# Performance work log

Hardware: AMD Instinct MI355X
Metric: run time of the kernel (lower is better)

## Reference

```python
import jax, jax.numpy as jnp
import numpy as np
from jax.scipy.special import gammaln

# NQ_IN + 4 == 2*H is required because the two kernel=1, padding=1 convs grow the
# length axis by 4 and the following nn.Linear(2H, H) acts on the length axis.
B, NQ_IN, NK, QDIM, KDIM, H = 16, 2044, 1024, 80, 256, 1024


def setup_inputs() -> dict:
    ks = jax.random.split(jax.random.key(0), 14)
    s = 0.02
    return {
        "query": jax.random.normal(ks[0], (B, NQ_IN, QDIM), jnp.float32),
        "key": jax.random.normal(ks[1], (B, NK, KDIM), jnp.float32),
        "query_lens": jnp.full((B,), 2 * H, jnp.int32),
        "key_lens": jnp.full((B,), NK, jnp.int32),
        # query branch params (Conv1d k=1 stored as (out,in); Linear as (out,in))
        "qc1_w": jax.random.normal(ks[2], (2 * H, QDIM), jnp.float32) * s,
        "qc1_b": jax.random.normal(ks[3], (2 * H,), jnp.float32) * s,
        "qc2_w": jax.random.normal(ks[4], (2 * H, 2 * H), jnp.float32) * s,
        "qc2_b": jax.random.normal(ks[5], (2 * H,), jnp.float32) * s,
        "ql_w": jax.random.normal(ks[6], (H, 2 * H), jnp.float32) * s,
        "ql_b": jax.random.normal(ks[7], (H,), jnp.float32) * s,
        # key branch params
        "kc_w": jax.random.normal(ks[8], (H, KDIM, 3), jnp.float32) * s,
        "kc_b": jax.random.normal(ks[9], (H,), jnp.float32) * s,
        "kl1_w": jax.random.normal(ks[10], (2 * H, H), jnp.float32) * s,
        "kl1_b": jax.random.normal(ks[11], (2 * H,), jnp.float32) * s,
        "kl2_w": jax.random.normal(ks[12], (H, 2 * H), jnp.float32) * s,
        "kl2_b": jax.random.normal(ks[13], (H,), jnp.float32) * s,
    }


def _log_beta_binom(query_lens, key_lens, tq, tk):
    # Standard MAS beta-binomial alignment prior over a (tq, tk) grid.
    i = jnp.arange(tq, dtype=jnp.float32)[None, :, None]
    j = jnp.arange(tk, dtype=jnp.float32)[None, None, :]
    ql = query_lens.astype(jnp.float32)[:, None, None]
    kl = key_lens.astype(jnp.float32)[:, None, None]
    a = i + 1.0
    b = jnp.maximum(ql - i, 1.0)
    n = jnp.maximum(kl - 1.0, 0.0)
    nmj = jnp.maximum(n - j, 0.0)

    def betaln(x, y):
        return gammaln(x) + gammaln(y) - gammaln(x + y)

    logp = (gammaln(n + 1.0) - gammaln(j + 1.0) - gammaln(nmj + 1.0)
            + betaln(j + a, nmj + b) - betaln(a, b))
    valid = (i < ql) & (j < kl)
    return jnp.where(valid, logp, -1e9)


def _forward(query, key, query_lens, key_lens,
             qc1_w, qc1_b, qc2_w, qc2_b, ql_w, ql_b,
             kc_w, kc_b, kl1_w, kl1_b, kl2_w, kl2_b):
    # query branch: b n c -> b c n, two k=1/p=1 convs (pad length, pointwise), Linear over LENGTH axis
    q = jnp.transpose(query, (0, 2, 1))                       # (B, QDIM, NQ_IN)
    q = jnp.pad(q, ((0, 0), (0, 0), (1, 1)))
    q = jnp.einsum('bcn,oc->bon', q, qc1_w) + qc1_b[None, :, None]   # (B, 2H, NQ_IN+2)
    q = jnp.pad(q, ((0, 0), (0, 0), (1, 1)))
    q = jnp.einsum('bcn,oc->bon', q, qc2_w) + qc2_b[None, :, None]   # (B, 2H, 2H)
    q = jnp.einsum('bcn,hn->bch', q, ql_w) + ql_b                    # (B, 2H, H) Linear on length axis

    # key branch: b n c -> b c n, Conv1d k=3 p=1, then two Linears over LENGTH axis
    k = jnp.transpose(key, (0, 2, 1))                         # (B, KDIM, NK)
    k = jax.lax.conv_general_dilated(k, kc_w, (1,), ((1, 1),),
                                     dimension_numbers=('NCH', 'OIH', 'NCH'))
    k = k + kc_b[None, :, None]                               # (B, H, NK=H)
    k = jnp.einsum('bcn,on->bco', k, kl1_w) + kl1_b           # (B, H, 2H)
    k = jnp.einsum('bco,ho->bch', k, kl2_w) + kl2_b           # (B, H, H)

    # dist = -cdist(q, k), computed via the GEMM form (same as torch.cdist mm mode)
    sq = (jnp.sum(q * q, -1)[:, :, None] + jnp.sum(k * k, -1)[:, None, :]
          - 2.0 * jnp.einsum('bnd,bmd->bnm', q, k))           # (B, 2H, H)
    dist = -jnp.sqrt(jnp.maximum(sq, 1e-12))

    prior = _log_beta_binom(query_lens, key_lens, q.shape[1], k.shape[1])
    return jax.nn.log_softmax(dist + prior, axis=-1)


def reference(query, key, query_lens, key_lens,
              qc1_w, qc1_b, qc2_w, qc2_b, ql_w, ql_b,
              kc_w, kc_b, kl1_w, kl1_b, kl2_w, kl2_b):
    return _forward(query, key, query_lens, key_lens,
                    qc1_w, qc1_b, qc2_w, qc2_b, ql_w, ql_b,
                    kc_w, kc_b, kl1_w, kl1_b, kl2_w, kl2_b)
```

## Files before the change

### kernel.cpp

```cpp
#include <hip/hip_runtime.h>
#include <math.h>

typedef unsigned short u16;
typedef float floatx4 __attribute__((ext_vector_type(4)));
typedef __bf16 bf16x8 __attribute__((ext_vector_type(8)));

#define BB   16
#define TQ   2048
#define TK   1024
#define HH   1024
#define H2   2048
#define QD   80
#define QDP  128
#define KD   256
#define NQ   2044
#define NKEY 1024

__device__ __forceinline__ u16 f2bf(float f) {
  unsigned int u = __float_as_uint(f);
  u = u + 0x7fffu + ((u >> 16) & 1u);
  return (u16)(u >> 16);
}
__device__ __forceinline__ float bf2f(u16 s) {
  return __uint_as_float(((unsigned int)s) << 16);
}

__global__ __launch_bounds__(256) void prep_all_k(
    const float* __restrict__ qc2_w, const float* __restrict__ qc1_w,
    const float* __restrict__ kl2_w, const float* __restrict__ kl1_w,
    const float* __restrict__ query, const float* __restrict__ ql_w,
    const float* __restrict__ kc_w,
    u16* __restrict__ qc2w, u16* __restrict__ qc1T, u16* __restrict__ kl2w,
    u16* __restrict__ kl1T, u16* __restrict__ qT, u16* __restrict__ qlw2,
    u16* __restrict__ kcp, float* __restrict__ tbl)
{
  long b = blockIdx.x;
  const int t = threadIdx.x;
  if (b < 16384) {
    long i = b * 256 + t; qc2w[i] = f2bf(qc2_w[i]); return;
  }
  b -= 16384;
  if (b < 1024) {
    long i = b * 256 + t;
    int c = (int)(i / H2), r = (int)(i % H2);
    qc1T[i] = (c < QD) ? f2bf(qc1_w[(long)r * QD + c]) : (u16)0; return;
  }
  b -= 1024;
  if (b < 8192) {
    long i = b * 256 + t; kl2w[i] = f2bf(kl2_w[i]); return;
  }
  b -= 8192;
  if (b < 8192) {
    long i = b * 256 + t;
    int c = (int)(i / H2), r = (int)(i % H2);
    kl1T[i] = f2bf(kl1_w[(long)r * HH + c]); return;
  }
  b -= 8192;
  if (b < 16384) {
    long i = b * 256 + t;
    int n = (int)(i & 2047);
    long rem = i >> 11;
    int c = (int)(rem % QDP);
    int bb = (int)(rem / QDP);
    qT[i] = (c < QD && n < NQ) ? f2bf(query[((long)bb * NQ + n) * QD + c]) : (u16)0; return;
  }
  b -= 16384;
  if (b < 8192) {
    long i = b * 256 + t;
    int n = (int)(i & 2047);
    int h = (int)(i >> 11);
    qlw2[i] = (n < NQ) ? f2bf(ql_w[(long)h * H2 + n + 2]) : (u16)0; return;
  }
  b -= 8192;
  if (b < 3072) {
    long i = b * 256 + t;
    int r = (int)(i % 768);
    int o = (int)(i / 768);
    int tt = r >> 8, d = r & 255;
    kcp[i] = f2bf(kc_w[((long)o * KD + d) * 3 + tt]); return;
  }
  b -= 3072;
  { int i = (int)(b * 256 + t); if (i < 8192) tbl[i] = i ? (float)lgamma((double)i) : 0.0f; }
}

__global__ __launch_bounds__(256) void fold_bias_k(
    const float* __restrict__ qc2_w, const float* __restrict__ qc1_b, const float* __restrict__ qc2_b,
    const float* __restrict__ kl2_w, const float* __restrict__ kl1_b, const float* __restrict__ kl2_b,
    const float* __restrict__ ql_w,
    float* __restrict__ bqm, float* __restrict__ bkv, float* __restrict__ s1v, float* __restrict__ s0v)
{
  const int bid = blockIdx.x, t = threadIdx.x;
  float s = 0.f;
  if (bid < H2) {
    const float* row = qc2_w + (long)bid * H2;
    for (int k = t; k < H2; k += 256) s += row[k] * qc1_b[k];
  } else if (bid < H2 + HH) {
    const float* row = kl2_w + (long)(bid - H2) * H2;
    for (int k = t; k < H2; k += 256) s += row[k] * kl1_b[k];
  } else {
    const float* row = ql_w + (long)(bid - H2 - HH) * H2;
    for (int m = 1 + t; m <= H2 - 2; m += 256) s += row[m];
  }
  __shared__ float red[256];
  red[t] = s; __syncthreads();
  for (int st = 128; st > 0; st >>= 1) { if (t < st) red[t] += red[t + st]; __syncthreads(); }
  if (!t) {
    if (bid < H2) bqm[bid] = red[0] + qc2_b[bid];
    else if (bid < H2 + HH) bkv[bid - H2] = red[0] + kl2_b[bid - H2];
    else {
      int h = bid - H2 - HH;
      s1v[h] = red[0];
      s0v[h] = ql_w[(long)h * H2] + ql_w[(long)h * H2 + H2 - 1];
    }
  }
}

__global__ __launch_bounds__(256) void rownorm2_k(const u16* __restrict__ Q, const u16* __restrict__ K3,
                                                  float* __restrict__ qn, float* __restrict__ kn) {
  const long r = blockIdx.x;
  const int t = threadIdx.x;
  const u16* row = (r < (long)BB * TQ) ? (Q + r * 1024) : (K3 + (r - (long)BB * TQ) * 1024);
  uint2 v = reinterpret_cast<const uint2*>(row)[t];
  float a0 = bf2f((u16)(v.x & 0xffff)), a1 = bf2f((u16)(v.x >> 16));
  float a2 = bf2f((u16)(v.y & 0xffff)), a3 = bf2f((u16)(v.y >> 16));
  float s = a0 * a0 + a1 * a1 + a2 * a2 + a3 * a3;
  __shared__ float red[256];
  red[t] = s; __syncthreads();
  for (int st = 128; st > 0; st >>= 1) { if (t < st) red[t] += red[t + st]; __syncthreads(); }
  if (!t) {
    if (r < (long)BB * TQ) qn[r] = red[0];
    else kn[r - (long)BB * TQ] = red[0];
  }
}


__device__ __forceinline__ void gld_lds16(const u16* g, u16* l) {
  __builtin_amdgcn_global_load_lds((const __attribute__((address_space(1))) void*)g,
                                   (__attribute__((address_space(3))) void*)l, 16, 0, 0);
}

template<int OUTF32>
__global__ __launch_bounds__(256) void gemm_bt(
    const u16* __restrict__ A, const u16* __restrict__ B, void* __restrict__ Cv,
    int M, int N, int K, int lda, int ldb, int swap,
    long sA, long sB, long sC,
    const float* __restrict__ colb, const float* __restrict__ rowb,
    const float* __restrict__ r1m, const float* __restrict__ r1n,
    const float* __restrict__ r2m, const float* __restrict__ r2n)
{
  __shared__ __align__(16) u16 As[128 * 32];
  __shared__ __align__(16) u16 Bs[128 * 32];
  const int bz = blockIdx.z;
  const int tid  = threadIdx.x;
  const int lane = tid & 63;
  const int wv = tid >> 6;
  const int wm = ((tid >> 7) & 1) * 64;
  const int wn = ((tid >> 6) & 1) * 64;
  const int m0 = (swap ? blockIdx.x : blockIdx.y) * 128;
  const int n0 = (swap ? blockIdx.y : blockIdx.x) * 128;

  const int srow = wv * 32 + (lane >> 2);
  const int scol = (lane & 3) << 3;
  const u16* ga = A + bz * sA + (long)(m0 + srow) * lda + scol;
  const u16* gb = B + bz * sB + (long)(n0 + srow) * ldb + scol;
  u16* la0 = &As[(wv * 32) * 32];
  u16* la1 = &As[(wv * 32 + 16) * 32];
  u16* lb0 = &Bs[(wv * 32) * 32];
  u16* lb1 = &Bs[(wv * 32 + 16) * 32];
  const long a16 = (long)16 * lda;
  const long b16 = (long)16 * ldb;

  floatx4 acc[4][4];
#pragma unroll
  for (int a_ = 0; a_ < 4; a_++)
#pragma unroll
    for (int b_ = 0; b_ < 4; b_++) acc[a_][b_] = (floatx4){0.f, 0.f, 0.f, 0.f};

  const int fr = lane & 15;
  const int fk = (lane >> 4) << 3;

  for (int kb = 0; kb < K; kb += 32) {
    gld_lds16(ga,       la0);
    gld_lds16(ga + a16, la1);
    gld_lds16(gb,       lb0);
    gld_lds16(gb + b16, lb1);
    ga += 32; gb += 32;
    __syncthreads();
    bf16x8 af[4], bfr[4];
#pragma unroll
    for (int mi = 0; mi < 4; mi++)
      af[mi] = *reinterpret_cast<const bf16x8*>(&As[(wm + mi * 16 + fr) * 32 + fk]);
#pragma unroll
    for (int ni = 0; ni < 4; ni++)
      bfr[ni] = *reinterpret_cast<const bf16x8*>(&Bs[(wn + ni * 16 + fr) * 32 + fk]);
#pragma unroll
    for (int mi = 0; mi < 4; mi++)
#pragma unroll
      for (int ni = 0; ni < 4; ni++)
        acc[mi][ni] = __builtin_amdgcn_mfma_f32_16x16x32_bf16(af[mi], bfr[ni], acc[mi][ni], 0, 0, 0);
    __syncthreads();
  }

  const int fr4 = (lane >> 4) << 2;
  const int fc  = lane & 15;
  u16*   Cb16 = (u16*)Cv + (long)bz * sC;
  float* Cb32 = (float*)Cv + (long)bz * sC;
#pragma unroll
  for (int mi = 0; mi < 4; mi++) {
#pragma unroll
    for (int ni = 0; ni < 4; ni++) {
      const int gm0 = m0 + wm + mi * 16 + fr4;
      const int gn  = n0 + wn + ni * 16 + fc;
      const float cbv  = colb ? colb[gn] : 0.f;
      const float r1nv = r1n ? r1n[gn] : 0.f;
      const float r2nv = r2n ? r2n[gn] : 0.f;
#pragma unroll
      for (int rr = 0; rr < 4; rr++) {
        const int gm = gm0 + rr;
        float v = acc[mi][ni][rr] + cbv;
        if (rowb) v += rowb[gm];
        if (r1m)  v += r1m[gm] * r1nv;
        if (r2m)  v += r2m[gm] * r2nv;
        if (OUTF32) Cb32[(long)gm * N + gn] = v;
        else        Cb16[(long)gm * N + gn] = f2bf(v);
      }
    }
  }
}

__global__ __launch_bounds__(256) void reduce_sk_k(const float* __restrict__ P, u16* __restrict__ out,
                                                   long MN, int S) {
  long i = ((long)blockIdx.x * 256 + threadIdx.x) * 4;
  if (i >= MN) return;
  float4 s = *reinterpret_cast<const float4*>(P + i);
  for (int t = 1; t < S; t++) {
    const float4 v = *reinterpret_cast<const float4*>(P + (long)t * MN + i);
    s.x += v.x; s.y += v.y; s.z += v.z; s.w += v.w;
  }
  union { u16 h[4]; uint2 u; } o;
  o.h[0] = f2bf(s.x); o.h[1] = f2bf(s.y); o.h[2] = f2bf(s.z); o.h[3] = f2bf(s.w);
  *reinterpret_cast<uint2*>(out + i) = o.u;
}

__global__ __launch_bounds__(256) void pack_im2col_k(const float* __restrict__ key, u16* __restrict__ out) {
  long i = (long)blockIdx.x * 256 + threadIdx.x;
  if (i >= (long)BB * NKEY * 768) return;
  int r = (int)(i % 768);
  long rem = i / 768;
  int n = (int)(rem % NKEY);
  int b = (int)(rem / NKEY);
  int t = r >> 8, d = r & 255;
  int src = n + t - 1;
  out[i] = (src >= 0 && src < NKEY) ? f2bf(key[((long)b * NKEY + src) * KD + d]) : (u16)0;
}

__global__ __launch_bounds__(256) void finalize_k(
    const u16* __restrict__ S, const float* __restrict__ qn, const float* __restrict__ kn,
    const int* __restrict__ qlens, const int* __restrict__ klens,
    const float* __restrict__ tbl, float* __restrict__ out)
{
  const int i = blockIdx.x;
  const int b = blockIdx.y;
  const int tid = threadIdx.x;
  const long rowoff = ((long)b * TQ + i) * TK;
  const int ql = qlens[b], kl = klens[b];
  const int n_ = (kl - 1 > 0) ? kl - 1 : 0;
  const int bb = (ql - i > 1) ? ql - i : 1;
  const float qni = qn[b * TQ + i];
#define TG(x) tbl[((x) < 8191) ? (x) : 8191]
  const float Crow = TG(n_ + 1) + TG(i + 1 + bb) - TG(i + 1) - TG(bb);
  const bool ivalid = (i < ql);

  float v[4];
  float lmax = -3.4e38f;
#pragma unroll
  for (int l = 0; l < 4; l++) {
    const int j = tid + (l << 8);
    const float Sv = bf2f(S[rowoff + j]);
    const float sq = fmaxf(qni + kn[b * TK + j] - 2.0f * Sv, 1e-12f);
    const float dist = -sqrtf(sq);
    float lp;
    if (ivalid && j < kl) {
      const int nmj = (n_ - j > 0) ? n_ - j : 0;
      lp = Crow - TG(j + 1) - TG(nmj + 1) + TG(i + j + 1) + TG(nmj + bb) - TG(i + j + 1 + nmj + bb);
    } else {
      lp = -1e9f;
    }
    v[l] = dist + lp;
    lmax = fmaxf(lmax, v[l]);
  }
  __shared__ float red[256];
  red[tid] = lmax; __syncthreads();
  for (int s = 128; s > 0; s >>= 1) { if (tid < s) red[tid] = fmaxf(red[tid], red[tid + s]); __syncthreads(); }
  const float gmax = red[0]; __syncthreads();
  float lsum = 0.f;
#pragma unroll
  for (int l = 0; l < 4; l++) lsum += expf(v[l] - gmax);
  red[tid] = lsum; __syncthreads();
  for (int s = 128; s > 0; s >>= 1) { if (tid < s) red[tid] += red[tid + s]; __syncthreads(); }
  const float lse = gmax + logf(red[0]);
#pragma unroll
  for (int l = 0; l < 4; l++) out[rowoff + tid + (l << 8)] = v[l] - lse;
#undef TG
}

extern "C" void kernel_launch(void* const* d_in, const int* in_sizes, int n_in,
                              void* d_out, int out_size, void* d_ws, size_t ws_size,
                              hipStream_t stream)
{
  (void)in_sizes; (void)n_in; (void)out_size; (void)ws_size;
  const float* query = (const float*)d_in[0];
  const float* key   = (const float*)d_in[1];
  const int*   qlens = (const int*)d_in[2];
  const int*   klens = (const int*)d_in[3];
  const float* qc1_w = (const float*)d_in[4];
  const float* qc1_b = (const float*)d_in[5];
  const float* qc2_w = (const float*)d_in[6];
  const float* qc2_b = (const float*)d_in[7];
  const float* ql_w  = (const float*)d_in[8];
  const float* ql_b  = (const float*)d_in[9];
  const float* kc_w  = (const float*)d_in[10];
  const float* kc_b  = (const float*)d_in[11];
  const float* kl1_w = (const float*)d_in[12];
  const float* kl1_b = (const float*)d_in[13];
  const float* kl2_w = (const float*)d_in[14];
  const float* kl2_b = (const float*)d_in[15];

  size_t off = 0;
  char* ws = (char*)d_ws;
  auto alloc = [&](size_t bytes) -> char* {
    char* p = ws + off; off += (bytes + 255) & ~(size_t)255; return p;
  };
  u16* qc2w_bf = (u16*)alloc(2ull * H2 * H2);
  u16* qc1T_bf = (u16*)alloc(2ull * QDP * H2);
  u16* kl2w_bf = (u16*)alloc(2ull * HH * H2);
  u16* kl1T_bf = (u16*)alloc(2ull * HH * H2);
  u16* qT_bf   = (u16*)alloc(2ull * BB * QDP * 2048);
  u16* kcol_bf = (u16*)d_ws;
  u16* S_bf    = (u16*)d_ws;
  u16* qlw2_bf = (u16*)alloc(2ull * HH * 2048);
  u16* kcp_bf  = (u16*)alloc(2ull * HH * 768);
  u16* Tp_bf   = (u16*)alloc(2ull * HH * 2048);
  u16* K1_bf   = (u16*)alloc(2ull * BB * HH * NKEY);
  float* Pbuf  = (float*)K1_bf;
  float* tbl  = (float*)alloc(4ull * 8192);
  u16* Wq_bf  = (u16*)alloc(2ull * H2 * QDP);
  u16* Wk_bf  = (u16*)alloc(2ull * HH * NKEY);
  float* bqm  = (float*)alloc(4ull * H2);
  float* bkv  = (float*)alloc(4ull * HH);
  float* s1v  = (float*)alloc(4ull * HH);
  float* s0v  = (float*)alloc(4ull * HH);
  u16* K3_bf  = (u16*)alloc(2ull * BB * TK * HH);
  float* qnv  = (float*)alloc(4ull * BB * TQ);
  float* knv  = (float*)alloc(4ull * BB * TK);
  u16* Q_bf   = (u16*)d_out;

  prep_all_k<<<61472, 256, 0, stream>>>(qc2_w, qc1_w, kl2_w, kl1_w, query, ql_w, kc_w,
                                        qc2w_bf, qc1T_bf, kl2w_bf, kl1T_bf, qT_bf, qlw2_bf, kcp_bf, tbl);
  fold_bias_k<<<4096, 256, 0, stream>>>(qc2_w, qc1_b, qc2_b, kl2_w, kl1_b, kl2_b, ql_w,
                                        bqm, bkv, s1v, s0v);

  gemm_bt<1><<<dim3(1, 16, 16), 256, 0, stream>>>(qc2w_bf, qc1T_bf, Pbuf, H2, QDP, 128,
      H2, H2, 0, 128, 128, (long)H2 * QDP,
      nullptr, nullptr, nullptr, nullptr, nullptr, nullptr);
  reduce_sk_k<<<256, 256, 0, stream>>>(Pbuf, Wq_bf, (long)H2 * QDP, 16);

  gemm_bt<1><<<dim3(8, 8, 8), 256, 0, stream>>>(kl2w_bf, kl1T_bf, Pbuf, HH, NKEY, 256,
      H2, H2, 0, 256, 256, (long)HH * NKEY,
      nullptr, nullptr, nullptr, nullptr, nullptr, nullptr);
  reduce_sk_k<<<1024, 256, 0, stream>>>(Pbuf, Wk_bf, (long)HH * NKEY, 8);

  gemm_bt<1><<<dim3(16, 8, 4), 256, 0, stream>>>(qlw2_bf, qT_bf, Pbuf, HH, 2048, 512,
      2048, 2048, 0, 512, 512, (long)HH * 2048,
      nullptr, nullptr, nullptr, nullptr, nullptr, nullptr);
  reduce_sk_k<<<2048, 256, 0, stream>>>(Pbuf, Tp_bf, (long)HH * 2048, 4);

  gemm_bt<0><<<dim3(8, 16, BB), 256, 0, stream>>>(Wq_bf, Tp_bf, Q_bf, H2, HH, QDP,
      QDP, 2048, 0, 0, 128, (long)TQ * HH,
      ql_b, nullptr, bqm, s1v, qc2_b, s0v);

  pack_im2col_k<<<(unsigned)(((long)BB * NKEY * 768 + 255) / 256), 256, 0, stream>>>(key, kcol_bf);
  gemm_bt<0><<<dim3(8, 8, BB), 256, 0, stream>>>(kcp_bf, kcol_bf, K1_bf, HH, NKEY, 768,
      768, 768, 0, 0, (long)NKEY * 768, (long)HH * NKEY,
      nullptr, kc_b, nullptr, nullptr, nullptr, nullptr);
  gemm_bt<0><<<dim3(8, 8, BB), 256, 0, stream>>>(K1_bf, Wk_bf, K3_bf, HH, NKEY, NKEY,
      NKEY, NKEY, 1, (long)HH * NKEY, 0, (long)TK * HH,
      bkv, nullptr, nullptr, nullptr, nullptr, nullptr);

  rownorm2_k<<<BB * TQ + BB * TK, 256, 0, stream>>>(Q_bf, K3_bf, qnv, knv);

  gemm_bt<0><<<dim3(16, 8, BB), 256, 0, stream>>>(Q_bf, K3_bf, S_bf, TQ, TK, HH,
      HH, HH, 1, (long)TQ * HH, (long)TK * HH, (long)TQ * TK,
      nullptr, nullptr, nullptr, nullptr, nullptr, nullptr);

  finalize_k<<<dim3(TQ, BB, 1), 256, 0, stream>>>(S_bf, qnv, knv, qlens, klens, tbl, (float*)d_out);
}
```

Baseline: 716.3 us.

## Reassociate query-key score GEMM through low-rank query factorization

Q is Wq·Tp plus rank-one bias terms, and the inner dimension of that product is 128. The large Q·K3ᵀ GEMM (K=1024) is therefore replaced by first computing Z = K3·Tp (per batch, N=128) and then S = Wq·Zᵀ with K=128, with the bias terms folded in through per-key dot products. Q is never materialized. Its row norms are instead computed algebraically from a per-batch Gram matrix TpᵀTp and several vector dot products. This removes the dominant 16×2048×1024×1024 GEMM and the Q write and read, at the cost of extra small kernels and bf16 rounding of the intermediates Z and G, which may affect accuracy.

```diff
diff --git a/kernel.cpp b/kernel.cpp
--- a/kernel.cpp
+++ b/kernel.cpp
@@ -115,25 +115,6 @@
   }
 }
 
-__global__ __launch_bounds__(256) void rownorm2_k(const u16* __restrict__ Q, const u16* __restrict__ K3,
-                                                  float* __restrict__ qn, float* __restrict__ kn) {
-  const long r = blockIdx.x;
-  const int t = threadIdx.x;
-  const u16* row = (r < (long)BB * TQ) ? (Q + r * 1024) : (K3 + (r - (long)BB * TQ) * 1024);
-  uint2 v = reinterpret_cast<const uint2*>(row)[t];
-  float a0 = bf2f((u16)(v.x & 0xffff)), a1 = bf2f((u16)(v.x >> 16));
-  float a2 = bf2f((u16)(v.y & 0xffff)), a3 = bf2f((u16)(v.y >> 16));
-  float s = a0 * a0 + a1 * a1 + a2 * a2 + a3 * a3;
-  __shared__ float red[256];
-  red[t] = s; __syncthreads();
-  for (int st = 128; st > 0; st >>= 1) { if (t < st) red[t] += red[t + st]; __syncthreads(); }
-  if (!t) {
-    if (r < (long)BB * TQ) qn[r] = red[0];
-    else kn[r - (long)BB * TQ] = red[0];
-  }
-}
-
-
 __device__ __forceinline__ void gld_lds16(const u16* g, u16* l) {
   __builtin_amdgcn_global_load_lds((const __attribute__((address_space(1))) void*)g,
                                    (__attribute__((address_space(3))) void*)l, 16, 0, 0);
@@ -142,8 +123,8 @@
 template<int OUTF32>
 __global__ __launch_bounds__(256) void gemm_bt(
     const u16* __restrict__ A, const u16* __restrict__ B, void* __restrict__ Cv,
-    int M, int N, int K, int lda, int ldb, int swap,
-    long sA, long sB, long sC,
+    int M, int N, int K, int lda, int ldb, int swap, int kspl,
+    long sA, long sB, long sC, long sN,
     const float* __restrict__ colb, const float* __restrict__ rowb,
     const float* __restrict__ r1m, const float* __restrict__ r1n,
     const float* __restrict__ r2m, const float* __restrict__ r2n)
@@ -151,6 +132,8 @@
   __shared__ __align__(16) u16 As[128 * 32];
   __shared__ __align__(16) u16 Bs[128 * 32];
   const int bz = blockIdx.z;
+  const int bb_ = (kspl > 1) ? bz / kspl : bz;
+  const int ks_ = (kspl > 1) ? bz - bb_ * kspl : 0;
   const int tid  = threadIdx.x;
   const int lane = tid & 63;
   const int wv = tid >> 6;
@@ -161,8 +144,8 @@
 
   const int srow = wv * 32 + (lane >> 2);
   const int scol = (lane & 3) << 3;
-  const u16* ga = A + bz * sA + (long)(m0 + srow) * lda + scol;
-  const u16* gb = B + bz * sB + (long)(n0 + srow) * ldb + scol;
+  const u16* ga = A + bb_ * sA + (long)ks_ * K + (long)(m0 + srow) * lda + scol;
+  const u16* gb = B + bb_ * sB + (long)ks_ * K + (long)(n0 + srow) * ldb + scol;
   u16* la0 = &As[(wv * 32) * 32];
   u16* la1 = &As[(wv * 32 + 16) * 32];
   u16* lb0 = &Bs[(wv * 32) * 32];
@@ -205,15 +188,18 @@
   const int fc  = lane & 15;
   u16*   Cb16 = (u16*)Cv + (long)bz * sC;
   float* Cb32 = (float*)Cv + (long)bz * sC;
+  const float* cbp  = colb ? colb + (long)bb_ * sN : nullptr;
+  const float* r1np = r1n ? r1n + (long)bb_ * sN : nullptr;
+  const float* r2np = r2n ? r2n + (long)bb_ * sN : nullptr;
 #pragma unroll
   for (int mi = 0; mi < 4; mi++) {
 #pragma unroll
     for (int ni = 0; ni < 4; ni++) {
       const int gm0 = m0 + wm + mi * 16 + fr4;
       const int gn  = n0 + wn + ni * 16 + fc;
-      const float cbv  = colb ? colb[gn] : 0.f;
-      const float r1nv = r1n ? r1n[gn] : 0.f;
-      const float r2nv = r2n ? r2n[gn] : 0.f;
+      const float cbv  = cbp ? cbp[gn] : 0.f;
+      const float r1nv = r1np ? r1np[gn] : 0.f;
+      const float r2nv = r2np ? r2np[gn] : 0.f;
 #pragma unroll
       for (int rr = 0; rr < 4; rr++) {
         const int gm = gm0 + rr;
@@ -228,18 +214,20 @@
   }
 }
 
-__global__ __launch_bounds__(256) void reduce_sk_k(const float* __restrict__ P, u16* __restrict__ out,
-                                                   long MN, int S) {
-  long i = ((long)blockIdx.x * 256 + threadIdx.x) * 4;
-  if (i >= MN) return;
-  float4 s = *reinterpret_cast<const float4*>(P + i);
+__global__ __launch_bounds__(256) void reduce_bk_k(const float* __restrict__ P, u16* __restrict__ out,
+                                                   long chunk, int S, long total) {
+  long j = ((long)blockIdx.x * 256 + threadIdx.x) * 4;
+  if (j >= total) return;
+  long b = j / chunk;
+  const float* p = P + j + b * chunk * (S - 1);
+  float4 s = *reinterpret_cast<const float4*>(p);
   for (int t = 1; t < S; t++) {
-    const float4 v = *reinterpret_cast<const float4*>(P + (long)t * MN + i);
+    const float4 v = *reinterpret_cast<const float4*>(p + (long)t * chunk);
     s.x += v.x; s.y += v.y; s.z += v.z; s.w += v.w;
   }
   union { u16 h[4]; uint2 u; } o;
   o.h[0] = f2bf(s.x); o.h[1] = f2bf(s.y); o.h[2] = f2bf(s.z); o.h[3] = f2bf(s.w);
-  *reinterpret_cast<uint2*>(out + i) = o.u;
+  *reinterpret_cast<uint2*>(out + j) = o.u;
 }
 
 __global__ __launch_bounds__(256) void pack_im2col_k(const float* __restrict__ key, u16* __restrict__ out) {
@@ -252,6 +240,102 @@
   int t = r >> 8, d = r & 255;
   int src = n + t - 1;
   out[i] = (src >= 0 && src < NKEY) ? f2bf(key[((long)b * NKEY + src) * KD + d]) : (u16)0;
+}
+
+__global__ __launch_bounds__(256) void u_k(
+    const u16* __restrict__ TpT, const float* __restrict__ qlb,
+    const float* __restrict__ s1, const float* __restrict__ s0,
+    float* __restrict__ u0, float* __restrict__ u1, float* __restrict__ u2,
+    float* __restrict__ sc)
+{
+  const int bid = blockIdx.x, t = threadIdx.x;
+  __shared__ float4 red[256];
+  if (bid < BB * QDP) {
+    uint2 v = reinterpret_cast<const uint2*>(TpT + (long)bid * HH)[t];
+    float a0 = bf2f((u16)(v.x & 0xffff)), a1 = bf2f((u16)(v.x >> 16));
+    float a2 = bf2f((u16)(v.y & 0xffff)), a3 = bf2f((u16)(v.y >> 16));
+    float4 q  = reinterpret_cast<const float4*>(qlb)[t];
+    float4 w1 = reinterpret_cast<const float4*>(s1)[t];
+    float4 w0 = reinterpret_cast<const float4*>(s0)[t];
+    float4 s;
+    s.x = a0 * q.x  + a1 * q.y  + a2 * q.z  + a3 * q.w;
+    s.y = a0 * w1.x + a1 * w1.y + a2 * w1.z + a3 * w1.w;
+    s.z = a0 * w0.x + a1 * w0.y + a2 * w0.z + a3 * w0.w;
+    s.w = 0.f;
+    red[t] = s; __syncthreads();
+    for (int st = 128; st > 0; st >>= 1) {
+      if (t < st) { red[t].x += red[t + st].x; red[t].y += red[t + st].y; red[t].z += red[t + st].z; }
+      __syncthreads();
+    }
+    if (!t) { u0[bid] = red[0].x; u1[bid] = red[0].y; u2[bid] = red[0].z; }
+  } else {
+    const int idx = bid - BB * QDP;
+    const float* X = (idx == 1 || idx == 5) ? s1 : (idx == 2) ? s0 : qlb;
+    const float* Y = (idx == 1 || idx == 3) ? s1 : (idx == 0) ? qlb : s0;
+    float4 x = reinterpret_cast<const float4*>(X)[t];
+    float4 y = reinterpret_cast<const float4*>(Y)[t];
+    float4 s; s.x = x.x * y.x + x.y * y.y + x.z * y.z + x.w * y.w; s.y = s.z = s.w = 0.f;
+    red[t] = s; __syncthreads();
+    for (int st = 128; st > 0; st >>= 1) {
+      if (t < st) red[t].x += red[t + st].x;
+      __syncthreads();
+    }
+    if (!t) sc[idx] = red[0].x;
+  }
+}
+
+__global__ __launch_bounds__(256) void qn_k(
+    const u16* __restrict__ Wq, const float* __restrict__ WqG,
+    const float* __restrict__ u0, const float* __restrict__ u1, const float* __restrict__ u2,
+    const float* __restrict__ bqm, const float* __restrict__ qc2_b,
+    const float* __restrict__ sc, float* __restrict__ qn)
+{
+  const int bx = blockIdx.x, t = threadIdx.x;
+  const int b = bx >> 10;
+  const int i = ((bx & 1023) << 1) | (t >> 7);
+  const int d = t & 127;
+  const float w  = bf2f(Wq[(long)i * QDP + d]);
+  const float g  = WqG[((long)b * H2 + i) * QDP + d];
+  const float bq = bqm[i], q2 = qc2_b[i];
+  const float uu = u0[b * QDP + d] + bq * u1[b * QDP + d] + q2 * u2[b * QDP + d];
+  __shared__ float red[256];
+  red[t] = w * (g + 2.f * uu); __syncthreads();
+  for (int s = 64; s > 0; s >>= 1) { if ((t & 127) < s) red[t] += red[t + s]; __syncthreads(); }
+  if (d == 0) {
+    const float cst = sc[0] + bq * bq * sc[1] + q2 * q2 * sc[2]
+                    + 2.f * (bq * sc[3] + q2 * sc[4] + bq * q2 * sc[5]);
+    qn[b * TQ + i] = red[t] + cst;
+  }
+}
+
+__global__ __launch_bounds__(256) void rownormk_k(
+    const u16* __restrict__ K3, const float* __restrict__ qlb,
+    const float* __restrict__ s1, const float* __restrict__ s0,
+    float* __restrict__ kn, float* __restrict__ yb, float* __restrict__ y1, float* __restrict__ y0)
+{
+  const long r = blockIdx.x;
+  const int t = threadIdx.x;
+  uint2 v = reinterpret_cast<const uint2*>(K3 + r * HH)[t];
+  float a0 = bf2f((u16)(v.x & 0xffff)), a1 = bf2f((u16)(v.x >> 16));
+  float a2 = bf2f((u16)(v.y & 0xffff)), a3 = bf2f((u16)(v.y >> 16));
+  float4 q  = reinterpret_cast<const float4*>(qlb)[t];
+  float4 w1 = reinterpret_cast<const float4*>(s1)[t];
+  float4 w0 = reinterpret_cast<const float4*>(s0)[t];
+  float4 s;
+  s.x = a0 * a0   + a1 * a1   + a2 * a2   + a3 * a3;
+  s.y = a0 * q.x  + a1 * q.y  + a2 * q.z  + a3 * q.w;
+  s.z = a0 * w1.x + a1 * w1.y + a2 * w1.z + a3 * w1.w;
+  s.w = a0 * w0.x + a1 * w0.y + a2 * w0.z + a3 * w0.w;
+  __shared__ float4 red[256];
+  red[t] = s; __syncthreads();
+  for (int st = 128; st > 0; st >>= 1) {
+    if (t < st) {
+      red[t].x += red[t + st].x; red[t].y += red[t + st].y;
+      red[t].z += red[t + st].z; red[t].w += red[t + st].w;
+    }
+    __syncthreads();
+  }
+  if (!t) { kn[r] = red[0].x; yb[r] = red[0].y; y1[r] = red[0].z; y0[r] = red[0].w; }
 }
 
 __global__ __launch_bounds__(256) void finalize_k(
@@ -340,7 +424,7 @@
   u16* S_bf    = (u16*)d_ws;
   u16* qlw2_bf = (u16*)alloc(2ull * HH * 2048);
   u16* kcp_bf  = (u16*)alloc(2ull * HH * 768);
-  u16* Tp_bf   = (u16*)alloc(2ull * HH * 2048);
+  u16* TpT_bf  = (u16*)alloc(2ull * H2 * HH);
   u16* K1_bf   = (u16*)alloc(2ull * BB * HH * NKEY);
   float* Pbuf  = (float*)K1_bf;
   float* tbl  = (float*)alloc(4ull * 8192);
@@ -353,7 +437,16 @@
   u16* K3_bf  = (u16*)alloc(2ull * BB * TK * HH);
   float* qnv  = (float*)alloc(4ull * BB * TQ);
   float* knv  = (float*)alloc(4ull * BB * TK);
-  u16* Q_bf   = (u16*)d_out;
+  float* ybv  = (float*)alloc(4ull * BB * TK);
+  float* y1v  = (float*)alloc(4ull * BB * TK);
+  float* y0v  = (float*)alloc(4ull * BB * TK);
+  float* u0v  = (float*)alloc(4ull * BB * QDP);
+  float* u1v  = (float*)alloc(4ull * BB * QDP);
+  float* u2v  = (float*)alloc(4ull * BB * QDP);
+  float* scv  = (float*)alloc(256);
+  float* WqG  = (float*)d_out;
+  u16* G_bf   = (u16*)((char*)d_out + 16777216);
+  u16* Z2_bf  = (u16*)((char*)d_out + 16777216 + 524288);
 
   prep_all_k<<<61472, 256, 0, stream>>>(qc2_w, qc1_w, kl2_w, kl1_w, query, ql_w, kc_w,
                                         qc2w_bf, qc1T_bf, kl2w_bf, kl1T_bf, qT_bf, qlw2_bf, kcp_bf, tbl);
@@ -361,37 +454,49 @@
                                         bqm, bkv, s1v, s0v);
 
   gemm_bt<1><<<dim3(1, 16, 16), 256, 0, stream>>>(qc2w_bf, qc1T_bf, Pbuf, H2, QDP, 128,
-      H2, H2, 0, 128, 128, (long)H2 * QDP,
+      H2, H2, 0, 16, 0, 0, (long)H2 * QDP, 0,
       nullptr, nullptr, nullptr, nullptr, nullptr, nullptr);
-  reduce_sk_k<<<256, 256, 0, stream>>>(Pbuf, Wq_bf, (long)H2 * QDP, 16);
+  reduce_bk_k<<<256, 256, 0, stream>>>(Pbuf, Wq_bf, (long)H2 * QDP, 16, (long)H2 * QDP);
 
   gemm_bt<1><<<dim3(8, 8, 8), 256, 0, stream>>>(kl2w_bf, kl1T_bf, Pbuf, HH, NKEY, 256,
-      H2, H2, 0, 256, 256, (long)HH * NKEY,
+      H2, H2, 0, 8, 0, 0, (long)HH * NKEY, 0,
       nullptr, nullptr, nullptr, nullptr, nullptr, nullptr);
-  reduce_sk_k<<<1024, 256, 0, stream>>>(Pbuf, Wk_bf, (long)HH * NKEY, 8);
-
-  gemm_bt<1><<<dim3(16, 8, 4), 256, 0, stream>>>(qlw2_bf, qT_bf, Pbuf, HH, 2048, 512,
-      2048, 2048, 0, 512, 512, (long)HH * 2048,
+  reduce_bk_k<<<1024, 256, 0, stream>>>(Pbuf, Wk_bf, (long)HH * NKEY, 8, (long)HH * NKEY);
+
+  gemm_bt<1><<<dim3(8, 16, 4), 256, 0, stream>>>(qT_bf, qlw2_bf, Pbuf, H2, HH, 512,
+      2048, 2048, 0, 4, 0, 0, (long)H2 * HH, 0,
       nullptr, nullptr, nullptr, nullptr, nullptr, nullptr);
-  reduce_sk_k<<<2048, 256, 0, stream>>>(Pbuf, Tp_bf, (long)HH * 2048, 4);
-
-  gemm_bt<0><<<dim3(8, 16, BB), 256, 0, stream>>>(Wq_bf, Tp_bf, Q_bf, H2, HH, QDP,
-      QDP, 2048, 0, 0, 128, (long)TQ * HH,
-      ql_b, nullptr, bqm, s1v, qc2_b, s0v);
+  reduce_bk_k<<<2048, 256, 0, stream>>>(Pbuf, TpT_bf, (long)H2 * HH, 4, (long)H2 * HH);
+
+  gemm_bt<1><<<dim3(1, 1, 128), 256, 0, stream>>>(TpT_bf, TpT_bf, Pbuf, 128, 128, 128,
+      HH, HH, 0, 8, (long)QDP * HH, (long)QDP * HH, 128 * 128, 0,
+      nullptr, nullptr, nullptr, nullptr, nullptr, nullptr);
+  reduce_bk_k<<<256, 256, 0, stream>>>(Pbuf, G_bf, 128 * 128, 8, (long)BB * 128 * 128);
+
+  gemm_bt<1><<<dim3(1, 16, 16), 256, 0, stream>>>(Wq_bf, G_bf, WqG, H2, QDP, QDP,
+      QDP, QDP, 0, 1, 0, (long)QDP * QDP, (long)H2 * QDP, 0,
+      nullptr, nullptr, nullptr, nullptr, nullptr, nullptr);
+  u_k<<<BB * QDP + 6, 256, 0, stream>>>(TpT_bf, ql_b, s1v, s0v, u0v, u1v, u2v, scv);
+  qn_k<<<BB * TQ / 2, 256, 0, stream>>>(Wq_bf, WqG, u0v, u1v, u2v, bqm, qc2_b, scv, qnv);
 
   pack_im2col_k<<<(unsigned)(((long)BB * NKEY * 768 + 255) / 256), 256, 0, stream>>>(key, kcol_bf);
   gemm_bt<0><<<dim3(8, 8, BB), 256, 0, stream>>>(kcp_bf, kcol_bf, K1_bf, HH, NKEY, 768,
-      768, 768, 0, 0, (long)NKEY * 768, (long)HH * NKEY,
+      768, 768, 0, 1, 0, (long)NKEY * 768, (long)HH * NKEY, 0,
       nullptr, kc_b, nullptr, nullptr, nullptr, nullptr);
   gemm_bt<0><<<dim3(8, 8, BB), 256, 0, stream>>>(K1_bf, Wk_bf, K3_bf, HH, NKEY, NKEY,
-      NKEY, NKEY, 1, (long)HH * NKEY, 0, (long)TK * HH,
+      NKEY, NKEY, 1, 1, (long)HH * NKEY, 0, (long)TK * HH, 0,
       bkv, nullptr, nullptr, nullptr, nullptr, nullptr);
 
-  rownorm2_k<<<BB * TQ + BB * TK, 256, 0, stream>>>(Q_bf, K3_bf, qnv, knv);
-
-  gemm_bt<0><<<dim3(16, 8, BB), 256, 0, stream>>>(Q_bf, K3_bf, S_bf, TQ, TK, HH,
-      HH, HH, 1, (long)TQ * HH, (long)TK * HH, (long)TQ * TK,
+  gemm_bt<1><<<dim3(8, 1, 32), 256, 0, stream>>>(K3_bf, TpT_bf, Pbuf, TK, QDP, 512,
+      HH, HH, 1, 2, (long)TK * HH, (long)QDP * HH, (long)TK * QDP, 0,
       nullptr, nullptr, nullptr, nullptr, nullptr, nullptr);
+  reduce_bk_k<<<2048, 256, 0, stream>>>(Pbuf, Z2_bf, (long)TK * QDP, 2, (long)BB * TK * QDP);
+
+  rownormk_k<<<BB * TK, 256, 0, stream>>>(K3_bf, ql_b, s1v, s0v, knv, ybv, y1v, y0v);
+
+  gemm_bt<0><<<dim3(8, 16, BB), 256, 0, stream>>>(Wq_bf, Z2_bf, S_bf, H2, TK, QDP,
+      QDP, QDP, 0, 1, 0, (long)TK * QDP, (long)TQ * TK, (long)TK,
+      ybv, nullptr, bqm, y1v, qc2_b, y0v);
 
   finalize_k<<<dim3(TQ, BB, 1), 256, 0, stream>>>(S_bf, qnv, knv, qlens, klens, tbl, (float*)d_out);
 }
```

Result: faster. 671.0 us (-6.3%).
